# Kernel optimization log

Hardware: AMD Instinct MI355X
Metric: run time of the kernel (lower is better)

The kernel has to match this reference:

```python
import jax, jax.numpy as jnp
import numpy as np

N, E, G = 40000, 640000, 64
D, H, O = 128, 128, 10
EPS = 1e-5


def _lin(k, fan_in, shape):
    b = 1.0 / np.sqrt(fan_in)
    return jax.random.uniform(k, shape, jnp.float32, -b, b)


def setup_inputs() -> dict:
    key = jax.random.key(0)
    ks = jax.random.split(key, 12)
    x = jax.random.normal(ks[0], (N, D), jnp.float32)
    edge_index = jax.random.randint(ks[1], (2, E), 0, N)
    batch = jnp.sort(jax.random.randint(ks[2], (N,), 0, G))
    return {
        "x": x,
        "edge_index": edge_index,
        "batch": batch,
        "num_graphs": G,
        "W_gcn": _lin(ks[3], D, (D, H)),
        "b_gcn": jnp.zeros((H,), jnp.float32),
        "gamma": jnp.ones((H,), jnp.float32),
        "beta": jnp.zeros((H,), jnp.float32),
        "W1": _lin(ks[4], 3 * H, (3 * H, H)),
        "b1": _lin(ks[5], 3 * H, (H,)),
        "W2": _lin(ks[6], H, (H, H // 2)),
        "b2": _lin(ks[7], H, (H // 2,)),
        "W3": _lin(ks[8], H // 2, (H // 2, O)),
        "b3": _lin(ks[9], H // 2, (O,)),
    }


def reference(x, edge_index, batch, num_graphs, W_gcn, b_gcn, gamma, beta, W1, b1, W2, b2, W3, b3):
    n = x.shape[0]
    src, dst = edge_index[0], edge_index[1]
    # GCNConv: h = D^{-1/2} (A + I) D^{-1/2} (x W) + b  (self-loops, symmetric norm)
    h = x @ W_gcn                                   # [N, H]
    deg = jax.ops.segment_sum(jnp.ones((src.shape[0],), h.dtype), dst, num_segments=n) + 1.0
    dinv = jax.lax.rsqrt(deg)                       # [N]
    coef = dinv[src] * dinv[dst]                    # [E]
    msg = h[src] * coef[:, None]                    # [E, H] gather (memory bound)
    agg = jax.ops.segment_sum(msg, dst, num_segments=n)
    agg = agg + h * (dinv * dinv)[:, None] + b_gcn  # self-loop term + bias
    h = jax.nn.relu(agg)
    # LayerNorm over feature dim
    mu = jnp.mean(h, axis=-1, keepdims=True)
    var = jnp.mean(jnp.square(h - mu), axis=-1, keepdims=True)
    h = (h - mu) * jax.lax.rsqrt(var + EPS) * gamma + beta
    # global mean / add / max pools keyed by graph id
    counts = jax.ops.segment_sum(jnp.ones((n,), h.dtype), batch, num_segments=num_graphs)
    x_add = jax.ops.segment_sum(h, batch, num_segments=num_graphs)
    x_mean = x_add / jnp.maximum(counts, 1.0)[:, None]
    x_max = jax.ops.segment_max(h, batch, num_segments=num_graphs)
    x_max = jnp.where(counts[:, None] > 0, x_max, 0.0)
    g = jnp.concatenate([x_mean, x_add, x_max], axis=1)  # [G, 3H]
    # MLP head (dropout is identity at inference)
    g = jax.nn.relu(g @ W1 + b1)
    g = jax.nn.relu(g @ W2 + b2)
    return g @ W3 + b3
```

## Files before the change

### kernel.cpp

```cpp
#include <hip/hip_runtime.h>
#include <math.h>

#define EPS 1e-5f
#define FLT_BIG 3.402823466e38f

typedef __attribute__((ext_vector_type(8))) short bf16x8;
typedef __attribute__((ext_vector_type(4))) float f32x4;

__device__ __forceinline__ unsigned fflip(float f){
  int i = __float_as_int(f);
  return (unsigned)(i ^ ((i>>31) | 0x80000000));
}
__device__ __forceinline__ float funflip(unsigned u){
  int i = (u & 0x80000000u) ? (int)(u ^ 0x80000000u) : (int)(~u);
  return __int_as_float(i);
}
__device__ __forceinline__ unsigned f2bf(float f){
  unsigned u = __float_as_uint(f);
  return (u + 0x7FFFu + ((u>>16)&1u)) >> 16;
}
__device__ __forceinline__ float bf_lo(unsigned v){ return __uint_as_float(v<<16); }
__device__ __forceinline__ float bf_hi(unsigned v){ return __uint_as_float(v & 0xFFFF0000u); }

__device__ __forceinline__ int lbound(const int* __restrict__ a, int n, int key){
  int lo=0, hi=n;
  while(lo<hi){ int mid=(lo+hi)>>1; if(a[mid]<key) lo=mid+1; else hi=mid; }
  return lo;
}

__global__ __launch_bounds__(256) void k_init(
    const float4* __restrict__ x4, int nq, uint2* __restrict__ xb2,
    int* __restrict__ cursor, int N,
    unsigned* __restrict__ psum, unsigned* __restrict__ pmaxu, int GP,
    const float* __restrict__ Wg, ushort* __restrict__ Wp){
  int i = blockIdx.x*blockDim.x + threadIdx.x;
  if(i<nq){
    float4 v = x4[i];
    uint2 o;
    o.x = (f2bf(v.y)<<16) | f2bf(v.x);
    o.y = (f2bf(v.w)<<16) | f2bf(v.z);
    xb2[i] = o;
  }
  if(i<N) cursor[i] = i<<6;
  if(i<GP){ psum[i]=0u; pmaxu[i]=0u; }
  if(i<2048){
    int tile = i>>6, l = i&63;
    int kt = tile>>3, ct = tile&7;
    int q = l>>4, nn = l&15;
    ushort w8[8];
    #pragma unroll
    for(int j=0;j<8;j++)
      w8[j] = (ushort)f2bf(Wg[(kt*32 + q*8 + j)*128 + ct*16 + nn]);
    ushort* dst = Wp + (size_t)i*8;
    #pragma unroll
    for(int j=0;j<8;j++) dst[j] = w8[j];
  }
}

__global__ void k_scatter(const int* __restrict__ src, const int* __restrict__ dst, int E,
                          int* __restrict__ cursor, int* __restrict__ csr){
  int e = blockIdx.x*blockDim.x + threadIdx.x;
  if(e<E){
    int d = dst[e];
    int p = atomicAdd(&cursor[d],1);
    if(p < (d<<6)+64) csr[p] = src[e];
  }
}

__global__ void k_agg(const unsigned* __restrict__ xb, const int* __restrict__ cursor,
                      const int* __restrict__ csr, int n, unsigned* __restrict__ zb){
  int w = (blockIdx.x*blockDim.x + threadIdx.x)>>6;
  int lane = threadIdx.x & 63;
  if(w>=n) return;
  int k0 = w<<6;
  int deg = cursor[w] - k0; if(deg>64) deg=64;
  float dd = rsqrtf((float)deg + 1.0f);
  int k1 = k0 + deg;
  unsigned xv = xb[k0 + lane];
  float sc = dd*dd;
  float ax = bf_lo(xv)*sc, ay = bf_hi(xv)*sc;
  int k = k0;
  for(; k+3 < k1; k+=4){
    int s0=csr[k], s1=csr[k+1], s2=csr[k+2], s3=csr[k+3];
    int d0=cursor[s0]-(s0<<6), d1=cursor[s1]-(s1<<6);
    int d2=cursor[s2]-(s2<<6), d3=cursor[s3]-(s3<<6);
    if(d0>64)d0=64; if(d1>64)d1=64; if(d2>64)d2=64; if(d3>64)d3=64;
    float c0=rsqrtf((float)d0+1.f)*dd, c1=rsqrtf((float)d1+1.f)*dd;
    float c2=rsqrtf((float)d2+1.f)*dd, c3=rsqrtf((float)d3+1.f)*dd;
    unsigned v0=xb[(s0<<6)+lane], v1=xb[(s1<<6)+lane];
    unsigned v2=xb[(s2<<6)+lane], v3=xb[(s3<<6)+lane];
    ax += c0*bf_lo(v0); ay += c0*bf_hi(v0);
    ax += c1*bf_lo(v1); ay += c1*bf_hi(v1);
    ax += c2*bf_lo(v2); ay += c2*bf_hi(v2);
    ax += c3*bf_lo(v3); ay += c3*bf_hi(v3);
  }
  for(; k<k1; k++){
    int s=csr[k];
    int ds_=cursor[s]-(s<<6); if(ds_>64)ds_=64;
    float c = rsqrtf((float)ds_+1.f)*dd;
    unsigned v=xb[(s<<6)+lane];
    ax += c*bf_lo(v); ay += c*bf_hi(v);
  }
  zb[(w<<6)+lane] = (f2bf(ay)<<16) | f2bf(ax);
}

__global__ __launch_bounds__(256) void k_gemmln(
    const unsigned* __restrict__ zb, const ushort* __restrict__ Wp,
    const float* __restrict__ bgc, const float* __restrict__ gamma, const float* __restrict__ beta,
    const int* __restrict__ batch, int n,
    float* __restrict__ pool_sum, unsigned* __restrict__ pool_maxu){
  __shared__ unsigned ztu[64*68];
  int t = threadIdx.x, lane = t & 63, wv = t >> 6;
  int rowBase = blockIdx.x*64;
  {
    int row = t>>2, qo = (t&3)*16;
    unsigned* lp = ztu + row*68 + qo;
    if(rowBase+row < n){
      const uint4* gp = (const uint4*)(zb + (size_t)(rowBase+row)*64 + qo);
      #pragma unroll
      for(int i=0;i<4;i++) ((uint4*)lp)[i] = gp[i];
    }else{
      #pragma unroll
      for(int i=0;i<4;i++) ((uint4*)lp)[i] = make_uint4(0,0,0,0);
    }
  }
  __syncthreads();

  int q = lane>>4, nn = lane&15;
  int m = wv*16 + nn;
  bf16x8 afr[4];
  #pragma unroll
  for(int kt=0;kt<4;kt++)
    afr[kt] = *(const bf16x8*)((const char*)ztu + m*272 + kt*64 + q*16);

  f32x4 acc[8];
  #pragma unroll
  for(int ct=0;ct<8;ct++){
    f32x4 c = {0.f,0.f,0.f,0.f};
    #pragma unroll
    for(int kt=0;kt<4;kt++){
      bf16x8 bfr = *(const bf16x8*)(Wp + ((size_t)(kt*8+ct)*64 + lane)*8);
      c = __builtin_amdgcn_mfma_f32_16x16x32_bf16(afr[kt], bfr, c, 0, 0, 0);
    }
    acc[ct] = c;
  }
  float s[4]={0,0,0,0}, qq[4]={0,0,0,0};
  #pragma unroll
  for(int ct=0;ct<8;ct++){
    float bb = bgc[ct*16+nn];
    #pragma unroll
    for(int r=0;r<4;r++){
      float v = acc[ct][r] + bb;
      v = fmaxf(v, 0.f);
      acc[ct][r] = v;
      s[r] += v; qq[r] += v*v;
    }
  }
  #pragma unroll
  for(int d=1; d<16; d<<=1){
    #pragma unroll
    for(int r=0;r<4;r++){
      s[r]  += __shfl_xor(s[r],  d, 64);
      qq[r] += __shfl_xor(qq[r], d, 64);
    }
  }
  float mu[4], isd[4];
  #pragma unroll
  for(int r=0;r<4;r++){
    mu[r] = s[r]*(1.f/128.f);
    float var = qq[r]*(1.f/128.f) - mu[r]*mu[r];
    isd[r] = rsqrtf(var + EPS);
  }
  #pragma unroll
  for(int ct=0;ct<8;ct++){
    float gm = gamma[ct*16+nn], bt = beta[ct*16+nn];
    #pragma unroll
    for(int r=0;r<4;r++)
      acc[ct][r] = (acc[ct][r]-mu[r])*isd[r]*gm + bt;
  }
  int gbr[4];
  #pragma unroll
  for(int r=0;r<4;r++){
    int gr = rowBase + wv*16 + q*4 + r;
    gbr[r] = (gr < n) ? batch[gr] : -1;
  }
  int b0i = rowBase + wv*16; if(b0i >= n) b0i = n-1;
  int b15i = rowBase + wv*16 + 15; if(b15i >= n) b15i = n-1;
  int gmin = batch[b0i], gmax = batch[b15i];
  if(gmax < gmin) gmax = gmin;
  for(int g=gmin; g<=gmax; ++g){
    #pragma unroll
    for(int ct=0;ct<8;ct++){
      float ssum = 0.f, smax = -FLT_BIG;
      #pragma unroll
      for(int r=0;r<4;r++){
        if(gbr[r]==g){
          ssum += acc[ct][r];
          smax = fmaxf(smax, acc[ct][r]);
        }
      }
      ssum += __shfl_xor(ssum, 16, 64);
      ssum += __shfl_xor(ssum, 32, 64);
      float o1 = __shfl_xor(smax, 16, 64); smax = fmaxf(smax, o1);
      float o2 = __shfl_xor(smax, 32, 64); smax = fmaxf(smax, o2);
      if(q==0){
        if(ssum != 0.f)   atomicAdd(&pool_sum[g*128 + ct*16 + nn], ssum);
        if(smax > -FLT_BIG) atomicMax(&pool_maxu[g*128 + ct*16 + nn], fflip(smax));
      }
    }
  }
}

__global__ void k_head(const float* __restrict__ pool_sum, const unsigned* __restrict__ pool_maxu,
                       const int* __restrict__ batch, int n,
                       const float* __restrict__ W1, const float* __restrict__ b1,
                       const float* __restrict__ W2, const float* __restrict__ b2,
                       const float* __restrict__ W3, const float* __restrict__ b3,
                       float* __restrict__ out){
  int g = blockIdx.x, t = threadIdx.x;
  __shared__ float red[2][128];
  __shared__ float gl[384];
  __shared__ float h1[128];
  __shared__ float h2[64];
  __shared__ int cnt_s;
  if(t==0){
    int s = lbound(batch,n,g), e = lbound(batch,n,g+1);
    cnt_s = e - s;
  }
  __syncthreads();
  int cnt = cnt_s;
  if(t<128){
    float s = pool_sum[g*128+t];
    gl[128+t] = s;
    gl[t] = s / (float)((cnt>1)?cnt:1);
    float m = funflip(pool_maxu[g*128+t]);
    gl[256+t] = (cnt>0) ? m : 0.f;
  }
  __syncthreads();
  int j = t & 127, kh = t >> 7;
  float p=0.f;
  for(int k=kh*192; k<kh*192+192; k++) p += gl[k]*W1[k*128+j];
  red[kh][j]=p;
  __syncthreads();
  if(t<128){
    float v = red[0][t]+red[1][t]+b1[t];
    h1[t]=fmaxf(v,0.f);
  }
  __syncthreads();
  if(t<64){
    float a=b2[t];
    for(int k=0;k<128;k++) a += h1[k]*W2[k*64+t];
    h2[t]=fmaxf(a,0.f);
  }
  __syncthreads();
  if(t<10){
    float a=b3[t];
    for(int k=0;k<64;k++) a += h2[k]*W3[k*10+t];
    out[g*10+t]=a;
  }
}

extern "C" void kernel_launch(void* const* d_in, const int* in_sizes, int n_in,
                              void* d_out, int out_size, void* d_ws, size_t ws_size,
                              hipStream_t stream){
  const float* x     = (const float*)d_in[0];
  const int*   ei    = (const int*)d_in[1];
  const int*   batch = (const int*)d_in[2];
  const float* Wg    = (const float*)d_in[4];
  const float* bg    = (const float*)d_in[5];
  const float* gamma = (const float*)d_in[6];
  const float* beta  = (const float*)d_in[7];
  const float* W1    = (const float*)d_in[8];
  const float* b1    = (const float*)d_in[9];
  const float* W2    = (const float*)d_in[10];
  const float* b2    = (const float*)d_in[11];
  const float* W3    = (const float*)d_in[12];
  const float* b3    = (const float*)d_in[13];
  float* out = (float*)d_out;

  int N = in_sizes[0]/128;
  int E = in_sizes[1]/2;
  const int G = 64;
  const int* src = ei;
  const int* dst = ei + E;

  char* p = (char*)d_ws;
  auto alloc=[&](size_t bytes)->char*{ char* r=p; p += (bytes+255)&~(size_t)255; return r; };
  int*      cursor = (int*)     alloc((size_t)N*4);
  int*      csr    = (int*)     alloc((size_t)N*64*4);
  unsigned* zb     = (unsigned*)alloc((size_t)N*64*4);
  float*    psum   = (float*)   alloc((size_t)G*128*4);
  unsigned* pmaxu  = (unsigned*)alloc((size_t)G*128*4);
  unsigned* xb     = (unsigned*)alloc((size_t)N*64*4);
  ushort*   Wp     = (ushort*)  alloc(2048*8*2);

  int GP = G*128;
  int nq = N*32;
  int ib = (nq+255)/256;
  k_init<<<ib,256,0,stream>>>((const float4*)x,nq,(uint2*)xb,cursor,N,
                              (unsigned*)psum,pmaxu,GP,Wg,Wp);
  int eb = (E+255)/256;
  k_scatter<<<eb,256,0,stream>>>(src,dst,E,cursor,csr);
  int ab = (int)(((size_t)N*64 + 255)/256);
  k_agg<<<ab,256,0,stream>>>(xb,cursor,csr,N,zb);
  k_gemmln<<<(N+63)/64,256,0,stream>>>(zb,Wp,bg,gamma,beta,batch,N,psum,pmaxu);
  k_head<<<G,256,0,stream>>>(psum,pmaxu,batch,N,W1,b1,W2,b2,W3,b3,out);
}
```

Baseline: 183.6 us.

## Pre-scale features by inverse sqrt degree and widen neighbour gathers in aggregation

```diff
diff --git a/kernel.cpp b/kernel.cpp
--- a/kernel.cpp
+++ b/kernel.cpp
@@ -29,19 +29,11 @@
 }
 
 __global__ __launch_bounds__(256) void k_init(
-    const float4* __restrict__ x4, int nq, uint2* __restrict__ xb2,
     int* __restrict__ cursor, int N,
     unsigned* __restrict__ psum, unsigned* __restrict__ pmaxu, int GP,
     const float* __restrict__ Wg, ushort* __restrict__ Wp){
   int i = blockIdx.x*blockDim.x + threadIdx.x;
-  if(i<nq){
-    float4 v = x4[i];
-    uint2 o;
-    o.x = (f2bf(v.y)<<16) | f2bf(v.x);
-    o.y = (f2bf(v.w)<<16) | f2bf(v.z);
-    xb2[i] = o;
-  }
-  if(i<N) cursor[i] = i<<6;
+  if(i<N) cursor[i] = 0;
   if(i<GP){ psum[i]=0u; pmaxu[i]=0u; }
   if(i<2048){
     int tile = i>>6, l = i&63;
@@ -59,49 +51,93 @@
 
 __global__ void k_scatter(const int* __restrict__ src, const int* __restrict__ dst, int E,
                           int* __restrict__ cursor, int* __restrict__ csr){
-  int e = blockIdx.x*blockDim.x + threadIdx.x;
-  if(e<E){
-    int d = dst[e];
-    int p = atomicAdd(&cursor[d],1);
-    if(p < (d<<6)+64) csr[p] = src[e];
-  }
-}
-
-__global__ void k_agg(const unsigned* __restrict__ xb, const int* __restrict__ cursor,
-                      const int* __restrict__ csr, int n, unsigned* __restrict__ zb){
+  int i = blockIdx.x*blockDim.x + threadIdx.x;
+  int e = i<<2;
+  if((E&3)==0){
+    if(e<E){
+      int4 s4 = *(const int4*)(src+e);
+      int4 d4 = *(const int4*)(dst+e);
+      int p;
+      p = atomicAdd(&cursor[d4.x],1); if(p<64) csr[(d4.x<<6)+p] = s4.x;
+      p = atomicAdd(&cursor[d4.y],1); if(p<64) csr[(d4.y<<6)+p] = s4.y;
+      p = atomicAdd(&cursor[d4.z],1); if(p<64) csr[(d4.z<<6)+p] = s4.z;
+      p = atomicAdd(&cursor[d4.w],1); if(p<64) csr[(d4.w<<6)+p] = s4.w;
+    }
+  } else {
+    #pragma unroll
+    for(int j=0;j<4;j++){
+      int ee = e+j;
+      if(ee<E){
+        int s = src[ee], d = dst[ee];
+        int p = atomicAdd(&cursor[d],1);
+        if(p<64) csr[(d<<6)+p] = s;
+      }
+    }
+  }
+}
+
+__global__ __launch_bounds__(256) void k_scale(
+    const float4* __restrict__ x4, int nq, const int* __restrict__ cursor,
+    uint2* __restrict__ xs2){
+  int i = blockIdx.x*blockDim.x + threadIdx.x;
+  if(i>=nq) return;
+  int node = i>>5;
+  int deg = cursor[node]; if(deg>64) deg=64;
+  float dinv = rsqrtf((float)deg + 1.0f);
+  float4 v = x4[i];
+  uint2 o;
+  o.x = (f2bf(v.y*dinv)<<16) | f2bf(v.x*dinv);
+  o.y = (f2bf(v.w*dinv)<<16) | f2bf(v.z*dinv);
+  xs2[i] = o;
+}
+
+__global__ void k_agg(const uint4* __restrict__ xs4, const int* __restrict__ cursor,
+                      const int* __restrict__ csr, int n, uint4* __restrict__ zb4){
   int w = (blockIdx.x*blockDim.x + threadIdx.x)>>6;
+  if(w>=n) return;
   int lane = threadIdx.x & 63;
-  if(w>=n) return;
-  int k0 = w<<6;
-  int deg = cursor[w] - k0; if(deg>64) deg=64;
+  int grp = lane>>4, li = lane&15;
+  int deg = cursor[w]; if(deg>64) deg=64;
+  int k0 = w<<6, k1 = k0+deg;
   float dd = rsqrtf((float)deg + 1.0f);
-  int k1 = k0 + deg;
-  unsigned xv = xb[k0 + lane];
-  float sc = dd*dd;
-  float ax = bf_lo(xv)*sc, ay = bf_hi(xv)*sc;
-  int k = k0;
-  for(; k+3 < k1; k+=4){
-    int s0=csr[k], s1=csr[k+1], s2=csr[k+2], s3=csr[k+3];
-    int d0=cursor[s0]-(s0<<6), d1=cursor[s1]-(s1<<6);
-    int d2=cursor[s2]-(s2<<6), d3=cursor[s3]-(s3<<6);
-    if(d0>64)d0=64; if(d1>64)d1=64; if(d2>64)d2=64; if(d3>64)d3=64;
-    float c0=rsqrtf((float)d0+1.f)*dd, c1=rsqrtf((float)d1+1.f)*dd;
-    float c2=rsqrtf((float)d2+1.f)*dd, c3=rsqrtf((float)d3+1.f)*dd;
-    unsigned v0=xb[(s0<<6)+lane], v1=xb[(s1<<6)+lane];
-    unsigned v2=xb[(s2<<6)+lane], v3=xb[(s3<<6)+lane];
-    ax += c0*bf_lo(v0); ay += c0*bf_hi(v0);
-    ax += c1*bf_lo(v1); ay += c1*bf_hi(v1);
-    ax += c2*bf_lo(v2); ay += c2*bf_hi(v2);
-    ax += c3*bf_lo(v3); ay += c3*bf_hi(v3);
-  }
-  for(; k<k1; k++){
-    int s=csr[k];
-    int ds_=cursor[s]-(s<<6); if(ds_>64)ds_=64;
-    float c = rsqrtf((float)ds_+1.f)*dd;
-    unsigned v=xb[(s<<6)+lane];
-    ax += c*bf_lo(v); ay += c*bf_hi(v);
-  }
-  zb[(w<<6)+lane] = (f2bf(ay)<<16) | f2bf(ax);
+  float a0=0.f,a1=0.f,a2=0.f,a3=0.f,a4=0.f,a5=0.f,a6=0.f,a7=0.f;
+  if(grp==0){
+    uint4 sv = xs4[(w<<4)+li];
+    a0=bf_lo(sv.x); a1=bf_hi(sv.x); a2=bf_lo(sv.y); a3=bf_hi(sv.y);
+    a4=bf_lo(sv.z); a5=bf_hi(sv.z); a6=bf_lo(sv.w); a7=bf_hi(sv.w);
+  }
+  for(int kb=k0; kb<k1; kb+=16){
+    int base = kb + (grp<<2);
+    int4 s4 = *(const int4*)(csr + base);
+    if(base   < k1){ uint4 v = xs4[(s4.x<<4)+li];
+      a0+=bf_lo(v.x); a1+=bf_hi(v.x); a2+=bf_lo(v.y); a3+=bf_hi(v.y);
+      a4+=bf_lo(v.z); a5+=bf_hi(v.z); a6+=bf_lo(v.w); a7+=bf_hi(v.w); }
+    if(base+1 < k1){ uint4 v = xs4[(s4.y<<4)+li];
+      a0+=bf_lo(v.x); a1+=bf_hi(v.x); a2+=bf_lo(v.y); a3+=bf_hi(v.y);
+      a4+=bf_lo(v.z); a5+=bf_hi(v.z); a6+=bf_lo(v.w); a7+=bf_hi(v.w); }
+    if(base+2 < k1){ uint4 v = xs4[(s4.z<<4)+li];
+      a0+=bf_lo(v.x); a1+=bf_hi(v.x); a2+=bf_lo(v.y); a3+=bf_hi(v.y);
+      a4+=bf_lo(v.z); a5+=bf_hi(v.z); a6+=bf_lo(v.w); a7+=bf_hi(v.w); }
+    if(base+3 < k1){ uint4 v = xs4[(s4.w<<4)+li];
+      a0+=bf_lo(v.x); a1+=bf_hi(v.x); a2+=bf_lo(v.y); a3+=bf_hi(v.y);
+      a4+=bf_lo(v.z); a5+=bf_hi(v.z); a6+=bf_lo(v.w); a7+=bf_hi(v.w); }
+  }
+  a0 += __shfl_xor(a0,16,64); a1 += __shfl_xor(a1,16,64);
+  a2 += __shfl_xor(a2,16,64); a3 += __shfl_xor(a3,16,64);
+  a4 += __shfl_xor(a4,16,64); a5 += __shfl_xor(a5,16,64);
+  a6 += __shfl_xor(a6,16,64); a7 += __shfl_xor(a7,16,64);
+  a0 += __shfl_xor(a0,32,64); a1 += __shfl_xor(a1,32,64);
+  a2 += __shfl_xor(a2,32,64); a3 += __shfl_xor(a3,32,64);
+  a4 += __shfl_xor(a4,32,64); a5 += __shfl_xor(a5,32,64);
+  a6 += __shfl_xor(a6,32,64); a7 += __shfl_xor(a7,32,64);
+  if(grp==0){
+    uint4 o;
+    o.x = (f2bf(a1*dd)<<16) | f2bf(a0*dd);
+    o.y = (f2bf(a3*dd)<<16) | f2bf(a2*dd);
+    o.z = (f2bf(a5*dd)<<16) | f2bf(a4*dd);
+    o.w = (f2bf(a7*dd)<<16) | f2bf(a6*dd);
+    zb4[(w<<4)+li] = o;
+  }
 }
 
 __global__ __launch_bounds__(256) void k_gemmln(
@@ -291,18 +327,19 @@
   unsigned* zb     = (unsigned*)alloc((size_t)N*64*4);
   float*    psum   = (float*)   alloc((size_t)G*128*4);
   unsigned* pmaxu  = (unsigned*)alloc((size_t)G*128*4);
-  unsigned* xb     = (unsigned*)alloc((size_t)N*64*4);
+  unsigned* xs     = (unsigned*)alloc((size_t)N*64*4);
   ushort*   Wp     = (ushort*)  alloc(2048*8*2);
 
   int GP = G*128;
   int nq = N*32;
-  int ib = (nq+255)/256;
-  k_init<<<ib,256,0,stream>>>((const float4*)x,nq,(uint2*)xb,cursor,N,
-                              (unsigned*)psum,pmaxu,GP,Wg,Wp);
-  int eb = (E+255)/256;
+  int ib = (N+255)/256;
+  k_init<<<ib,256,0,stream>>>(cursor,N,(unsigned*)psum,pmaxu,GP,Wg,Wp);
+  int eb = (E/4 + 255)/256;
   k_scatter<<<eb,256,0,stream>>>(src,dst,E,cursor,csr);
+  int sb = (nq+255)/256;
+  k_scale<<<sb,256,0,stream>>>((const float4*)x,nq,cursor,(uint2*)xs);
   int ab = (int)(((size_t)N*64 + 255)/256);
-  k_agg<<<ab,256,0,stream>>>(xb,cursor,csr,N,zb);
+  k_agg<<<ab,256,0,stream>>>((const uint4*)xs,cursor,csr,N,(uint4*)zb);
   k_gemmln<<<(N+63)/64,256,0,stream>>>(zb,Wp,bg,gamma,beta,batch,N,psum,pmaxu);
   k_head<<<G,256,0,stream>>>(psum,pmaxu,batch,N,W1,b1,W2,b2,W3,b3,out);
 }
```

New measurement: 180.9 us. About the same (-1.5%).
